# Performance work log

Hardware: AMD Instinct MI355X
Metric: run time of the kernel (lower is better)

The kernel has to match this reference:

```python
import jax, jax.numpy as jnp
import numpy as np

N = 50000   # n_nodes (cells)
E = 800000  # n_edges (avg degree 16)
D = 128     # feature dim


def setup_inputs() -> dict:
    key = jax.random.key(0)
    ks = jax.random.split(key, 8)
    x = jax.random.normal(ks[0], (N, D), dtype=jnp.float32)
    src = jax.random.randint(ks[1], (E,), 0, N, dtype=jnp.int32)
    dst = jax.random.randint(ks[2], (E,), 0, N, dtype=jnp.int32)
    vals = jax.random.uniform(ks[3], (E,), dtype=jnp.float32)
    # GraphConvolution weight (dim -> dim), applied as x @ W
    W_gc = jax.random.normal(ks[4], (D, D), dtype=jnp.float32) / np.sqrt(D).astype(np.float32)
    b_gc = jnp.zeros((D,), jnp.float32)
    # linear2: nn.Linear(dim, dim) -> x @ W2.T + b2
    W2 = jax.random.normal(ks[5], (D, D), dtype=jnp.float32) / np.sqrt(D).astype(np.float32)
    b2 = jnp.zeros((D,), jnp.float32)
    return {"x": x, "vals": vals, "W_gc": W_gc, "b_gc": b_gc,
            "W2": W2, "b2": b2, "src": src, "dst": dst}


def reference(x, vals, W_gc, b_gc, W2, b2, src, dst):
    # GraphConvolution (dropout is identity in eval mode):
    #   support = x @ W + b ; out = relu(adj_sparse @ support)
    support = x @ W_gc + b_gc                         # [N, D]
    msg = support[src] * vals[:, None]                # gather rows, scale by edge weight
    agg = jax.ops.segment_sum(msg, dst, num_segments=N)  # SpMM via scatter-add
    x1 = jax.nn.relu(agg)                             # [N, D]
    # linear2 + dropout(eval=identity) + detached L2 row-normalize
    x2 = x1 @ W2.T + b2                               # [N, D]
    nrm = jax.lax.stop_gradient(
        jnp.sqrt(jnp.sum(x2 * x2, axis=1, keepdims=True)))
    return x2 / nrm
```

## Files before the change

### kernel.cpp

```cpp
#include <hip/hip_runtime.h>
#include <hip/hip_bf16.h>

#define N_NODES 50000
#define N_EDGES 800000
#define DIM     128
#define N_STRIPS (N_NODES / 16)
#define N_BKT    782
#define EDGE_CHUNKS 196
#define BCAP     1536
#define EBUF_CAP 1408
#define AGS      68
#define GEMM_BLOCKS ((N_STRIPS + 3) / 4)
#define FRONT_BLOCKS (GEMM_BLOCKS + EDGE_CHUNKS)

typedef short short8 __attribute__((ext_vector_type(8)));
typedef float floatx4 __attribute__((ext_vector_type(4)));

__device__ inline unsigned short f2bf(float f) {
    __hip_bfloat16 h = __float2bfloat16(f);
    return *reinterpret_cast<unsigned short*>(&h);
}

__global__ __launch_bounds__(256) void pre_pack(
    const float* __restrict__ W1, const float* __restrict__ W2,
    uint4* __restrict__ p1, uint4* __restrict__ p2, int* __restrict__ bcnt)
{
    const int blk = blockIdx.x;
    const int t   = threadIdx.x;
    if (blk < 8) {
        const int s    = blk * 256 + t;
        const int lane = s & 63;
        const int nt   = (s >> 6) & 7;
        const int ks   = s >> 9;
        const int m    = lane & 15;
        const int q    = lane >> 4;
        unsigned short e[8];
        #pragma unroll
        for (int j = 0; j < 8; ++j)
            e[j] = f2bf(W1[(ks * 32 + q * 8 + j) * DIM + nt * 16 + m]);
        uint4 o;
        o.x = (unsigned)e[0] | ((unsigned)e[1] << 16);
        o.y = (unsigned)e[2] | ((unsigned)e[3] << 16);
        o.z = (unsigned)e[4] | ((unsigned)e[5] << 16);
        o.w = (unsigned)e[6] | ((unsigned)e[7] << 16);
        p1[s] = o;
    } else if (blk < 16) {
        const int s    = (blk - 8) * 256 + t;
        const int lane = s & 63;
        const int nt   = (s >> 6) & 7;
        const int ks   = s >> 9;
        const int m    = lane & 15;
        const int q    = lane >> 4;
        const float4 f0 = *reinterpret_cast<const float4*>(&W2[(nt * 16 + m) * DIM + ks * 32 + q * 8]);
        const float4 f1 = *reinterpret_cast<const float4*>(&W2[(nt * 16 + m) * DIM + ks * 32 + q * 8 + 4]);
        unsigned short e[8];
        e[0] = f2bf(f0.x); e[1] = f2bf(f0.y); e[2] = f2bf(f0.z); e[3] = f2bf(f0.w);
        e[4] = f2bf(f1.x); e[5] = f2bf(f1.y); e[6] = f2bf(f1.z); e[7] = f2bf(f1.w);
        uint4 o;
        o.x = (unsigned)e[0] | ((unsigned)e[1] << 16);
        o.y = (unsigned)e[2] | ((unsigned)e[3] << 16);
        o.z = (unsigned)e[4] | ((unsigned)e[5] << 16);
        o.w = (unsigned)e[6] | ((unsigned)e[7] << 16);
        p2[s] = o;
    } else {
        for (int i = t; i < 800; i += 256) bcnt[i] = 0;
    }
}

__global__ __launch_bounds__(256) void front(
    const float* __restrict__ x, const float* __restrict__ bias,
    const int* __restrict__ src, const int* __restrict__ dst,
    const float* __restrict__ vals, const uint4* __restrict__ p1,
    unsigned short* __restrict__ support, int* __restrict__ bcnt,
    int2* __restrict__ bucketed)
{
    __shared__ int bh[800];
    __shared__ int rcur[800];
    const int t = threadIdx.x;

    if (blockIdx.x < EDGE_CHUNKS) {
        const int chunk = blockIdx.x;
        for (int i = t; i < 800; i += 256) bh[i] = 0;
        __syncthreads();
        const int base   = chunk * 4096;
        const int navail = min(4096, N_EDGES - base);
        const int4* d4 = reinterpret_cast<const int4*>(dst + base);
        #pragma unroll
        for (int i = 0; i < 4; ++i) {
            const int j = t + i * 256;
            if (j * 4 < navail) {
                const int4 d = d4[j];
                atomicAdd(&bh[d.x >> 6], 1);
                atomicAdd(&bh[d.y >> 6], 1);
                atomicAdd(&bh[d.z >> 6], 1);
                atomicAdd(&bh[d.w >> 6], 1);
            }
        }
        __syncthreads();
        for (int b = t; b < N_BKT; b += 256)
            rcur[b] = b * BCAP + atomicAdd(&bcnt[b], bh[b]);
        __syncthreads();
        const int4*   s4 = reinterpret_cast<const int4*>(src + base);
        const float4* v4 = reinterpret_cast<const float4*>(vals + base);
        #pragma unroll
        for (int i = 0; i < 4; ++i) {
            const int j = t + i * 256;
            if (j * 4 < navail) {
                const int4   s = s4[j];
                const int4   d = d4[j];
                const float4 v = v4[j];
                int p;
                p = atomicAdd(&rcur[d.x >> 6], 1);
                bucketed[p] = make_int2((s.x & 0xFFFF) | ((d.x & 63) << 16), __float_as_int(v.x));
                p = atomicAdd(&rcur[d.y >> 6], 1);
                bucketed[p] = make_int2((s.y & 0xFFFF) | ((d.y & 63) << 16), __float_as_int(v.y));
                p = atomicAdd(&rcur[d.z >> 6], 1);
                bucketed[p] = make_int2((s.z & 0xFFFF) | ((d.z & 63) << 16), __float_as_int(v.z));
                p = atomicAdd(&rcur[d.w >> 6], 1);
                bucketed[p] = make_int2((s.w & 0xFFFF) | ((d.w & 63) << 16), __float_as_int(v.w));
            }
        }
    } else {
        const int wave  = t >> 6;
        const int lane  = t & 63;
        const int strip = (blockIdx.x - EDGE_CHUNKS) * 4 + wave;
        if (strip >= N_STRIPS) return;
        const int m = lane & 15;
        const int q = lane >> 4;
        const int row = strip * 16 + m;

        short8 a[4];
        const float4* xr = reinterpret_cast<const float4*>(&x[(size_t)row * DIM]);
        #pragma unroll
        for (int ks = 0; ks < 4; ++ks) {
            const float4 f0 = xr[ks * 8 + q * 2];
            const float4 f1 = xr[ks * 8 + q * 2 + 1];
            short8 tt;
            tt[0] = (short)f2bf(f0.x); tt[1] = (short)f2bf(f0.y);
            tt[2] = (short)f2bf(f0.z); tt[3] = (short)f2bf(f0.w);
            tt[4] = (short)f2bf(f1.x); tt[5] = (short)f2bf(f1.y);
            tt[6] = (short)f2bf(f1.z); tt[7] = (short)f2bf(f1.w);
            a[ks] = tt;
        }

        floatx4 acc[8];
        #pragma unroll
        for (int nt = 0; nt < 8; ++nt) { acc[nt][0]=0.f; acc[nt][1]=0.f; acc[nt][2]=0.f; acc[nt][3]=0.f; }

        const short8* Bp = (const short8*)p1;
        #pragma unroll
        for (int ks = 0; ks < 4; ++ks) {
            #pragma unroll
            for (int nt = 0; nt < 8; ++nt) {
                const short8 bf = Bp[(ks * 8 + nt) * 64 + lane];
                acc[nt] = __builtin_amdgcn_mfma_f32_16x16x32_bf16(a[ks], bf, acc[nt], 0, 0, 0);
            }
        }

        #pragma unroll
        for (int nt = 0; nt < 8; ++nt) {
            const float bb = bias[nt * 16 + m];
            #pragma unroll
            for (int i = 0; i < 4; ++i) {
                const int r = strip * 16 + q * 4 + i;
                support[(size_t)r * DIM + nt * 16 + m] = f2bf(acc[nt][i] + bb);
            }
        }
    }
}

__global__ __launch_bounds__(256) void agg_gemm2(
    const unsigned int* __restrict__ sup, const int2* __restrict__ bucketed,
    const int* __restrict__ bcnt, const short8* __restrict__ Bp,
    const float* __restrict__ bias, float* __restrict__ out)
{
    __shared__ int2 ebuf[EBUF_CAP];
    __shared__ unsigned int agg[64 * AGS];
    __shared__ int cnt[64];
    __shared__ int coff[64];
    __shared__ int cur[64];

    const int b = blockIdx.x;
    const int t = threadIdx.x;
    int nE = bcnt[b];
    if (nE > EBUF_CAP) nE = EBUF_CAP;
    const int base = b * BCAP;

    if (t < 64) cnt[t] = 0;
    __syncthreads();
    for (int i = t; i < nE; i += 256)
        atomicAdd(&cnt[(bucketed[base + i].x >> 16) & 63], 1);
    __syncthreads();
    if (t < 64) coff[t] = cnt[t];
    __syncthreads();
    for (int off = 1; off < 64; off <<= 1) {
        int u = 0;
        if (t < 64 && t >= off) u = coff[t - off];
        __syncthreads();
        if (t < 64 && t >= off) coff[t] += u;
        __syncthreads();
    }
    if (t < 64) cur[t] = coff[t] - cnt[t];
    __syncthreads();
    for (int i = t; i < nE; i += 256) {
        const int2 e = bucketed[base + i];
        const int  n = (e.x >> 16) & 63;
        const int  p = atomicAdd(&cur[n], 1);
        ebuf[p] = e;
    }
    __syncthreads();

    const int w    = t >> 6;
    const int lane = t & 63;
    const int g    = lane >> 4;
    const int dl   = lane & 15;

    for (int nl = w * 16; nl < w * 16 + 16; ++nl) {
        const int end = cur[nl];
        const int c   = cnt[nl];
        const int beg = end - c;
        float acc[8];
        #pragma unroll
        for (int k = 0; k < 8; ++k) acc[k] = 0.f;

        const int nI = (c + 3) >> 2;
        auto step = [&](int it) {
            const int  idx = beg + it * 4 + g;
            const bool vld = idx < end;
            const int2 e   = ebuf[vld ? idx : beg];
            const float val = vld ? __int_as_float(e.y) : 0.f;
            const uint4 u = *reinterpret_cast<const uint4*>(
                &sup[(size_t)(e.x & 0xFFFF) * 64 + dl * 4]);
            acc[0] += __uint_as_float(u.x << 16)          * val;
            acc[1] += __uint_as_float(u.x & 0xffff0000u)  * val;
            acc[2] += __uint_as_float(u.y << 16)          * val;
            acc[3] += __uint_as_float(u.y & 0xffff0000u)  * val;
            acc[4] += __uint_as_float(u.z << 16)          * val;
            acc[5] += __uint_as_float(u.z & 0xffff0000u)  * val;
            acc[6] += __uint_as_float(u.w << 16)          * val;
            acc[7] += __uint_as_float(u.w & 0xffff0000u)  * val;
        };
        int it = 0;
        for (; it + 3 < nI; it += 4) { step(it); step(it+1); step(it+2); step(it+3); }
        for (; it < nI; ++it) step(it);

        #pragma unroll
        for (int k = 0; k < 8; ++k) {
            acc[k] += __shfl_xor(acc[k], 16);
            acc[k] += __shfl_xor(acc[k], 32);
        }
        if (dl == lane) {
            uint4 o;
            o.x = (unsigned)f2bf(fmaxf(acc[0],0.f)) | ((unsigned)f2bf(fmaxf(acc[1],0.f)) << 16);
            o.y = (unsigned)f2bf(fmaxf(acc[2],0.f)) | ((unsigned)f2bf(fmaxf(acc[3],0.f)) << 16);
            o.z = (unsigned)f2bf(fmaxf(acc[4],0.f)) | ((unsigned)f2bf(fmaxf(acc[5],0.f)) << 16);
            o.w = (unsigned)f2bf(fmaxf(acc[6],0.f)) | ((unsigned)f2bf(fmaxf(acc[7],0.f)) << 16);
            *reinterpret_cast<uint4*>(&agg[nl * AGS + dl * 4]) = o;
        }
    }
    __syncthreads();

    const int row0 = b * 64 + w * 16;
    if (row0 >= N_NODES) return;
    const int m = lane & 15;
    const int q = lane >> 4;

    short8 a[4];
    #pragma unroll
    for (int ks = 0; ks < 4; ++ks) {
        const uint4 t4 = *reinterpret_cast<const uint4*>(&agg[(w * 16 + m) * AGS + ks * 16 + q * 4]);
        a[ks] = *reinterpret_cast<const short8*>(&t4);
    }

    floatx4 acc[8];
    #pragma unroll
    for (int nt = 0; nt < 8; ++nt) { acc[nt][0]=0.f; acc[nt][1]=0.f; acc[nt][2]=0.f; acc[nt][3]=0.f; }

    #pragma unroll
    for (int ks = 0; ks < 4; ++ks) {
        #pragma unroll
        for (int nt = 0; nt < 8; ++nt) {
            const short8 bf = Bp[(ks * 8 + nt) * 64 + lane];
            acc[nt] = __builtin_amdgcn_mfma_f32_16x16x32_bf16(a[ks], bf, acc[nt], 0, 0, 0);
        }
    }

    #pragma unroll
    for (int nt = 0; nt < 8; ++nt) {
        const float bb = bias[nt * 16 + m];
        #pragma unroll
        for (int i = 0; i < 4; ++i) acc[nt][i] += bb;
    }

    float sq[4] = {0.f, 0.f, 0.f, 0.f};
    #pragma unroll
    for (int nt = 0; nt < 8; ++nt)
        #pragma unroll
        for (int i = 0; i < 4; ++i) sq[i] += acc[nt][i] * acc[nt][i];
    #pragma unroll
    for (int i = 0; i < 4; ++i) {
        #pragma unroll
        for (int mask = 1; mask < 16; mask <<= 1)
            sq[i] += __shfl_xor(sq[i], mask);
        sq[i] = 1.0f / sqrtf(sq[i]);
    }

    #pragma unroll
    for (int nt = 0; nt < 8; ++nt) {
        #pragma unroll
        for (int i = 0; i < 4; ++i) {
            const int r = row0 + q * 4 + i;
            out[(size_t)r * DIM + nt * 16 + m] = acc[nt][i] * sq[i];
        }
    }
}

extern "C" void kernel_launch(void* const* d_in, const int* in_sizes, int n_in,
                              void* d_out, int out_size, void* d_ws, size_t ws_size,
                              hipStream_t stream) {
    const float* x    = (const float*)d_in[0];
    const float* vals = (const float*)d_in[1];
    const float* W_gc = (const float*)d_in[2];
    const float* b_gc = (const float*)d_in[3];
    const float* W2   = (const float*)d_in[4];
    const float* b2   = (const float*)d_in[5];
    const int*   src  = (const int*)d_in[6];
    const int*   dst  = (const int*)d_in[7];

    float* out = (float*)d_out;

    const size_t SUP_B = (size_t)N_NODES * DIM * 2;
    const size_t BUK_B = (size_t)N_BKT * BCAP * 8;
    char* wsb = (char*)d_ws;
    unsigned short* support = (unsigned short*)wsb;
    int2* bucketed = (int2*)(wsb + SUP_B);
    int*  bcnt     = (int*)(wsb + SUP_B + BUK_B);
    uint4* pw1     = (uint4*)(wsb + SUP_B + BUK_B + 4096);
    uint4* pw2     = (uint4*)(wsb + SUP_B + BUK_B + 4096 + 32768);

    pre_pack<<<17, 256, 0, stream>>>(W_gc, W2, pw1, pw2, bcnt);

    front<<<FRONT_BLOCKS, 256, 0, stream>>>(
        x, b_gc, src, dst, vals, pw1, support, bcnt, bucketed);

    agg_gemm2<<<N_BKT, 256, 0, stream>>>(
        (const unsigned int*)support, bucketed, bcnt, (const short8*)pw2, b2, out);
}
```

Baseline: 148.4 us.

## Split SpMM gather into two feature-half kernels and stage support writes through LDS

The aggregation is split into two passes, each gathering only one 64-feature half of the bf16 support rows. The first pass writes its half to a global buffer, and the second computes its half and then runs the second GEMM. The intent is to halve the gathered working set per pass so it fits better in cache, and to process two nodes per wave with 8-lane groups for more memory-level parallelism. The first GEMM now stages its output tile in LDS so global stores are coalesced, and edge chunks are doubled to 8192 edges. In exchange the edge bucket sort is done twice, one more kernel is launched, and there is an extra global round trip for the first half of the aggregation.

```diff
diff --git a/kernel.cpp b/kernel.cpp
--- a/kernel.cpp
+++ b/kernel.cpp
@@ -6,12 +6,13 @@
 #define DIM     128
 #define N_STRIPS (N_NODES / 16)
 #define N_BKT    782
-#define EDGE_CHUNKS 196
+#define CHUNK_E  8192
+#define EDGE_CHUNKS ((N_EDGES + CHUNK_E - 1) / CHUNK_E)
 #define BCAP     1536
 #define EBUF_CAP 1408
-#define AGS      68
 #define GEMM_BLOCKS ((N_STRIPS + 3) / 4)
-#define FRONT_BLOCKS (GEMM_BLOCKS + EDGE_CHUNKS)
+#define FRONT_BLOCKS (EDGE_CHUNKS + GEMM_BLOCKS)
+#define SUP_ROWS 50048
 
 typedef short short8 __attribute__((ext_vector_type(8)));
 typedef float floatx4 __attribute__((ext_vector_type(4)));
@@ -19,6 +20,15 @@
 __device__ inline unsigned short f2bf(float f) {
     __hip_bfloat16 h = __float2bfloat16(f);
     return *reinterpret_cast<unsigned short*>(&h);
+}
+
+__device__ inline uint4 pack8_relu(const float a[8]) {
+    uint4 o;
+    o.x = (unsigned)f2bf(fmaxf(a[0],0.f)) | ((unsigned)f2bf(fmaxf(a[1],0.f)) << 16);
+    o.y = (unsigned)f2bf(fmaxf(a[2],0.f)) | ((unsigned)f2bf(fmaxf(a[3],0.f)) << 16);
+    o.z = (unsigned)f2bf(fmaxf(a[4],0.f)) | ((unsigned)f2bf(fmaxf(a[5],0.f)) << 16);
+    o.w = (unsigned)f2bf(fmaxf(a[6],0.f)) | ((unsigned)f2bf(fmaxf(a[7],0.f)) << 16);
+    return o;
 }
 
 __global__ __launch_bounds__(256) void pre_pack(
@@ -76,17 +86,18 @@
 {
     __shared__ int bh[800];
     __shared__ int rcur[800];
+    __shared__ unsigned short stg[64 * 136];
     const int t = threadIdx.x;
 
     if (blockIdx.x < EDGE_CHUNKS) {
         const int chunk = blockIdx.x;
         for (int i = t; i < 800; i += 256) bh[i] = 0;
         __syncthreads();
-        const int base   = chunk * 4096;
-        const int navail = min(4096, N_EDGES - base);
+        const int base   = chunk * CHUNK_E;
+        const int navail = min(CHUNK_E, N_EDGES - base);
         const int4* d4 = reinterpret_cast<const int4*>(dst + base);
         #pragma unroll
-        for (int i = 0; i < 4; ++i) {
+        for (int i = 0; i < 8; ++i) {
             const int j = t + i * 256;
             if (j * 4 < navail) {
                 const int4 d = d4[j];
@@ -103,7 +114,7 @@
         const int4*   s4 = reinterpret_cast<const int4*>(src + base);
         const float4* v4 = reinterpret_cast<const float4*>(vals + base);
         #pragma unroll
-        for (int i = 0; i < 4; ++i) {
+        for (int i = 0; i < 8; ++i) {
             const int j = t + i * 256;
             if (j * 4 < navail) {
                 const int4   s = s4[j];
@@ -121,61 +132,70 @@
             }
         }
     } else {
+        const int gb    = blockIdx.x - EDGE_CHUNKS;
         const int wave  = t >> 6;
         const int lane  = t & 63;
-        const int strip = (blockIdx.x - EDGE_CHUNKS) * 4 + wave;
-        if (strip >= N_STRIPS) return;
+        const int strip = gb * 4 + wave;
         const int m = lane & 15;
         const int q = lane >> 4;
-        const int row = strip * 16 + m;
-
-        short8 a[4];
-        const float4* xr = reinterpret_cast<const float4*>(&x[(size_t)row * DIM]);
-        #pragma unroll
-        for (int ks = 0; ks < 4; ++ks) {
-            const float4 f0 = xr[ks * 8 + q * 2];
-            const float4 f1 = xr[ks * 8 + q * 2 + 1];
-            short8 tt;
-            tt[0] = (short)f2bf(f0.x); tt[1] = (short)f2bf(f0.y);
-            tt[2] = (short)f2bf(f0.z); tt[3] = (short)f2bf(f0.w);
-            tt[4] = (short)f2bf(f1.x); tt[5] = (short)f2bf(f1.y);
-            tt[6] = (short)f2bf(f1.z); tt[7] = (short)f2bf(f1.w);
-            a[ks] = tt;
-        }
-
-        floatx4 acc[8];
-        #pragma unroll
-        for (int nt = 0; nt < 8; ++nt) { acc[nt][0]=0.f; acc[nt][1]=0.f; acc[nt][2]=0.f; acc[nt][3]=0.f; }
-
-        const short8* Bp = (const short8*)p1;
-        #pragma unroll
-        for (int ks = 0; ks < 4; ++ks) {
+        const bool valid = strip < N_STRIPS;
+
+        if (valid) {
+            const int row = strip * 16 + m;
+            short8 a[4];
+            const float4* xr = reinterpret_cast<const float4*>(&x[(size_t)row * DIM]);
+            #pragma unroll
+            for (int ks = 0; ks < 4; ++ks) {
+                const float4 f0 = xr[ks * 8 + q * 2];
+                const float4 f1 = xr[ks * 8 + q * 2 + 1];
+                short8 tt;
+                tt[0] = (short)f2bf(f0.x); tt[1] = (short)f2bf(f0.y);
+                tt[2] = (short)f2bf(f0.z); tt[3] = (short)f2bf(f0.w);
+                tt[4] = (short)f2bf(f1.x); tt[5] = (short)f2bf(f1.y);
+                tt[6] = (short)f2bf(f1.z); tt[7] = (short)f2bf(f1.w);
+                a[ks] = tt;
+            }
+
+            floatx4 acc[8];
+            #pragma unroll
+            for (int nt = 0; nt < 8; ++nt) { acc[nt][0]=0.f; acc[nt][1]=0.f; acc[nt][2]=0.f; acc[nt][3]=0.f; }
+
+            const short8* Bp = (const short8*)p1;
+            #pragma unroll
+            for (int ks = 0; ks < 4; ++ks) {
+                #pragma unroll
+                for (int nt = 0; nt < 8; ++nt) {
+                    const short8 bf = Bp[(ks * 8 + nt) * 64 + lane];
+                    acc[nt] = __builtin_amdgcn_mfma_f32_16x16x32_bf16(a[ks], bf, acc[nt], 0, 0, 0);
+                }
+            }
+
             #pragma unroll
             for (int nt = 0; nt < 8; ++nt) {
-                const short8 bf = Bp[(ks * 8 + nt) * 64 + lane];
-                acc[nt] = __builtin_amdgcn_mfma_f32_16x16x32_bf16(a[ks], bf, acc[nt], 0, 0, 0);
+                const float bb = bias[nt * 16 + m];
+                #pragma unroll
+                for (int i = 0; i < 4; ++i)
+                    stg[(wave * 16 + q * 4 + i) * 136 + nt * 16 + m] = f2bf(acc[nt][i] + bb);
             }
         }
-
-        #pragma unroll
-        for (int nt = 0; nt < 8; ++nt) {
-            const float bb = bias[nt * 16 + m];
-            #pragma unroll
-            for (int i = 0; i < 4; ++i) {
-                const int r = strip * 16 + q * 4 + i;
-                support[(size_t)r * DIM + nt * 16 + m] = f2bf(acc[nt][i] + bb);
-            }
-        }
-    }
-}
-
-__global__ __launch_bounds__(256) void agg_gemm2(
+        __syncthreads();
+        const size_t rbase = (size_t)gb * 64;
+        #pragma unroll
+        for (int k = 0; k < 4; ++k) {
+            const int chunk2 = t + k * 256;
+            const int lrow  = chunk2 >> 4;
+            const int piece = chunk2 & 15;
+            const uint4 v = *reinterpret_cast<const uint4*>(&stg[lrow * 136 + piece * 8]);
+            *reinterpret_cast<uint4*>(&support[(rbase + lrow) * DIM + piece * 8]) = v;
+        }
+    }
+}
+
+__global__ __launch_bounds__(256) void gather_h0(
     const unsigned int* __restrict__ sup, const int2* __restrict__ bucketed,
-    const int* __restrict__ bcnt, const short8* __restrict__ Bp,
-    const float* __restrict__ bias, float* __restrict__ out)
+    const int* __restrict__ bcnt, unsigned int* __restrict__ aggG)
 {
     __shared__ int2 ebuf[EBUF_CAP];
-    __shared__ unsigned int agg[64 * AGS];
     __shared__ int cnt[64];
     __shared__ int coff[64];
     __shared__ int cur[64];
@@ -210,52 +230,160 @@
     }
     __syncthreads();
 
-    const int w    = t >> 6;
-    const int lane = t & 63;
-    const int g    = lane >> 4;
-    const int dl   = lane & 15;
-
-    for (int nl = w * 16; nl < w * 16 + 16; ++nl) {
-        const int end = cur[nl];
-        const int c   = cnt[nl];
-        const int beg = end - c;
-        float acc[8];
-        #pragma unroll
-        for (int k = 0; k < 8; ++k) acc[k] = 0.f;
-
-        const int nI = (c + 3) >> 2;
-        auto step = [&](int it) {
-            const int  idx = beg + it * 4 + g;
-            const bool vld = idx < end;
-            const int2 e   = ebuf[vld ? idx : beg];
-            const float val = vld ? __int_as_float(e.y) : 0.f;
-            const uint4 u = *reinterpret_cast<const uint4*>(
-                &sup[(size_t)(e.x & 0xFFFF) * 64 + dl * 4]);
-            acc[0] += __uint_as_float(u.x << 16)          * val;
-            acc[1] += __uint_as_float(u.x & 0xffff0000u)  * val;
-            acc[2] += __uint_as_float(u.y << 16)          * val;
-            acc[3] += __uint_as_float(u.y & 0xffff0000u)  * val;
-            acc[4] += __uint_as_float(u.z << 16)          * val;
-            acc[5] += __uint_as_float(u.z & 0xffff0000u)  * val;
-            acc[6] += __uint_as_float(u.w << 16)          * val;
-            acc[7] += __uint_as_float(u.w & 0xffff0000u)  * val;
-        };
-        int it = 0;
-        for (; it + 3 < nI; it += 4) { step(it); step(it+1); step(it+2); step(it+3); }
-        for (; it < nI; ++it) step(it);
-
+    const int w = t >> 6, lane = t & 63;
+    const int g = lane >> 3, dl = lane & 7;
+    for (int j = 0; j < 8; ++j) {
+        const int nA = w * 16 + j, nB = nA + 8;
+        const int endA = cur[nA], cA = cnt[nA], begA = endA - cA;
+        const int endB = cur[nB], cB = cnt[nB], begB = endB - cB;
+        float aA[8] = {0.f,0.f,0.f,0.f,0.f,0.f,0.f,0.f};
+        float aB[8] = {0.f,0.f,0.f,0.f,0.f,0.f,0.f,0.f};
+        const int nI = max((cA + 7) >> 3, (cB + 7) >> 3);
+        #pragma unroll 2
+        for (int it = 0; it < nI; ++it) {
+            const int iA = begA + it * 8 + g;
+            const int iB = begB + it * 8 + g;
+            const bool vA = iA < endA, vB = iB < endB;
+            const int2 eA = ebuf[vA ? iA : 0];
+            const int2 eB = ebuf[vB ? iB : 0];
+            const float valA = vA ? __int_as_float(eA.y) : 0.f;
+            const float valB = vB ? __int_as_float(eB.y) : 0.f;
+            const int sA = vA ? (eA.x & 0xFFFF) : 0;
+            const int sB = vB ? (eB.x & 0xFFFF) : 0;
+            const uint4 uA = *reinterpret_cast<const uint4*>(&sup[(size_t)sA * 64 + dl * 4]);
+            const uint4 uB = *reinterpret_cast<const uint4*>(&sup[(size_t)sB * 64 + dl * 4]);
+            aA[0] += __uint_as_float(uA.x << 16)         * valA;
+            aA[1] += __uint_as_float(uA.x & 0xffff0000u) * valA;
+            aA[2] += __uint_as_float(uA.y << 16)         * valA;
+            aA[3] += __uint_as_float(uA.y & 0xffff0000u) * valA;
+            aA[4] += __uint_as_float(uA.z << 16)         * valA;
+            aA[5] += __uint_as_float(uA.z & 0xffff0000u) * valA;
+            aA[6] += __uint_as_float(uA.w << 16)         * valA;
+            aA[7] += __uint_as_float(uA.w & 0xffff0000u) * valA;
+            aB[0] += __uint_as_float(uB.x << 16)         * valB;
+            aB[1] += __uint_as_float(uB.x & 0xffff0000u) * valB;
+            aB[2] += __uint_as_float(uB.y << 16)         * valB;
+            aB[3] += __uint_as_float(uB.y & 0xffff0000u) * valB;
+            aB[4] += __uint_as_float(uB.z << 16)         * valB;
+            aB[5] += __uint_as_float(uB.z & 0xffff0000u) * valB;
+            aB[6] += __uint_as_float(uB.w << 16)         * valB;
+            aB[7] += __uint_as_float(uB.w & 0xffff0000u) * valB;
+        }
         #pragma unroll
         for (int k = 0; k < 8; ++k) {
-            acc[k] += __shfl_xor(acc[k], 16);
-            acc[k] += __shfl_xor(acc[k], 32);
-        }
-        if (dl == lane) {
-            uint4 o;
-            o.x = (unsigned)f2bf(fmaxf(acc[0],0.f)) | ((unsigned)f2bf(fmaxf(acc[1],0.f)) << 16);
-            o.y = (unsigned)f2bf(fmaxf(acc[2],0.f)) | ((unsigned)f2bf(fmaxf(acc[3],0.f)) << 16);
-            o.z = (unsigned)f2bf(fmaxf(acc[4],0.f)) | ((unsigned)f2bf(fmaxf(acc[5],0.f)) << 16);
-            o.w = (unsigned)f2bf(fmaxf(acc[6],0.f)) | ((unsigned)f2bf(fmaxf(acc[7],0.f)) << 16);
-            *reinterpret_cast<uint4*>(&agg[nl * AGS + dl * 4]) = o;
+            aA[k] += __shfl_xor(aA[k], 8);
+            aA[k] += __shfl_xor(aA[k], 16);
+            aA[k] += __shfl_xor(aA[k], 32);
+            aB[k] += __shfl_xor(aB[k], 8);
+            aB[k] += __shfl_xor(aB[k], 16);
+            aB[k] += __shfl_xor(aB[k], 32);
+        }
+        if (lane < 8) {
+            const uint4 oA = pack8_relu(aA);
+            const uint4 oB = pack8_relu(aB);
+            const int nodeA = b * 64 + nA;
+            const int nodeB = b * 64 + nB;
+            if (nodeA < N_NODES)
+                *reinterpret_cast<uint4*>(&aggG[(size_t)nodeA * 32 + lane * 4]) = oA;
+            if (nodeB < N_NODES)
+                *reinterpret_cast<uint4*>(&aggG[(size_t)nodeB * 32 + lane * 4]) = oB;
+        }
+    }
+}
+
+__global__ __launch_bounds__(256) void gather_h1_gemm2(
+    const unsigned int* __restrict__ sup, const int2* __restrict__ bucketed,
+    const int* __restrict__ bcnt, const unsigned int* __restrict__ aggG,
+    const short8* __restrict__ Bp, const float* __restrict__ bias,
+    float* __restrict__ out)
+{
+    __shared__ int2 ebuf[EBUF_CAP];
+    __shared__ unsigned int aggL[64 * 36];
+    __shared__ int cnt[64];
+    __shared__ int coff[64];
+    __shared__ int cur[64];
+
+    const int b = blockIdx.x;
+    const int t = threadIdx.x;
+    int nE = bcnt[b];
+    if (nE > EBUF_CAP) nE = EBUF_CAP;
+    const int base = b * BCAP;
+
+    if (t < 64) cnt[t] = 0;
+    __syncthreads();
+    for (int i = t; i < nE; i += 256)
+        atomicAdd(&cnt[(bucketed[base + i].x >> 16) & 63], 1);
+    __syncthreads();
+    if (t < 64) coff[t] = cnt[t];
+    __syncthreads();
+    for (int off = 1; off < 64; off <<= 1) {
+        int u = 0;
+        if (t < 64 && t >= off) u = coff[t - off];
+        __syncthreads();
+        if (t < 64 && t >= off) coff[t] += u;
+        __syncthreads();
+    }
+    if (t < 64) cur[t] = coff[t] - cnt[t];
+    __syncthreads();
+    for (int i = t; i < nE; i += 256) {
+        const int2 e = bucketed[base + i];
+        const int  n = (e.x >> 16) & 63;
+        const int  p = atomicAdd(&cur[n], 1);
+        ebuf[p] = e;
+    }
+    __syncthreads();
+
+    const int w = t >> 6, lane = t & 63;
+    const int g = lane >> 3, dl = lane & 7;
+    for (int j = 0; j < 8; ++j) {
+        const int nA = w * 16 + j, nB = nA + 8;
+        const int endA = cur[nA], cA = cnt[nA], begA = endA - cA;
+        const int endB = cur[nB], cB = cnt[nB], begB = endB - cB;
+        float aA[8] = {0.f,0.f,0.f,0.f,0.f,0.f,0.f,0.f};
+        float aB[8] = {0.f,0.f,0.f,0.f,0.f,0.f,0.f,0.f};
+        const int nI = max((cA + 7) >> 3, (cB + 7) >> 3);
+        #pragma unroll 2
+        for (int it = 0; it < nI; ++it) {
+            const int iA = begA + it * 8 + g;
+            const int iB = begB + it * 8 + g;
+            const bool vA = iA < endA, vB = iB < endB;
+            const int2 eA = ebuf[vA ? iA : 0];
+            const int2 eB = ebuf[vB ? iB : 0];
+            const float valA = vA ? __int_as_float(eA.y) : 0.f;
+            const float valB = vB ? __int_as_float(eB.y) : 0.f;
+            const int sA = vA ? (eA.x & 0xFFFF) : 0;
+            const int sB = vB ? (eB.x & 0xFFFF) : 0;
+            const uint4 uA = *reinterpret_cast<const uint4*>(&sup[(size_t)sA * 64 + 32 + dl * 4]);
+            const uint4 uB = *reinterpret_cast<const uint4*>(&sup[(size_t)sB * 64 + 32 + dl * 4]);
+            aA[0] += __uint_as_float(uA.x << 16)         * valA;
+            aA[1] += __uint_as_float(uA.x & 0xffff0000u) * valA;
+            aA[2] += __uint_as_float(uA.y << 16)         * valA;
+            aA[3] += __uint_as_float(uA.y & 0xffff0000u) * valA;
+            aA[4] += __uint_as_float(uA.z << 16)         * valA;
+            aA[5] += __uint_as_float(uA.z & 0xffff0000u) * valA;
+            aA[6] += __uint_as_float(uA.w << 16)         * valA;
+            aA[7] += __uint_as_float(uA.w & 0xffff0000u) * valA;
+            aB[0] += __uint_as_float(uB.x << 16)         * valB;
+            aB[1] += __uint_as_float(uB.x & 0xffff0000u) * valB;
+            aB[2] += __uint_as_float(uB.y << 16)         * valB;
+            aB[3] += __uint_as_float(uB.y & 0xffff0000u) * valB;
+            aB[4] += __uint_as_float(uB.z << 16)         * valB;
+            aB[5] += __uint_as_float(uB.z & 0xffff0000u) * valB;
+            aB[6] += __uint_as_float(uB.w << 16)         * valB;
+            aB[7] += __uint_as_float(uB.w & 0xffff0000u) * valB;
+        }
+        #pragma unroll
+        for (int k = 0; k < 8; ++k) {
+            aA[k] += __shfl_xor(aA[k], 8);
+            aA[k] += __shfl_xor(aA[k], 16);
+            aA[k] += __shfl_xor(aA[k], 32);
+            aB[k] += __shfl_xor(aB[k], 8);
+            aB[k] += __shfl_xor(aB[k], 16);
+            aB[k] += __shfl_xor(aB[k], 32);
+        }
+        if (lane < 8) {
+            *reinterpret_cast<uint4*>(&aggL[nA * 36 + lane * 4]) = pack8_relu(aA);
+            *reinterpret_cast<uint4*>(&aggL[nB * 36 + lane * 4]) = pack8_relu(aB);
         }
     }
     __syncthreads();
@@ -264,11 +392,17 @@
     if (row0 >= N_NODES) return;
     const int m = lane & 15;
     const int q = lane >> 4;
+    const int grow = row0 + m;
 
     short8 a[4];
     #pragma unroll
-    for (int ks = 0; ks < 4; ++ks) {
-        const uint4 t4 = *reinterpret_cast<const uint4*>(&agg[(w * 16 + m) * AGS + ks * 16 + q * 4]);
+    for (int ks = 0; ks < 2; ++ks) {
+        const uint4 t4 = *reinterpret_cast<const uint4*>(&aggG[(size_t)grow * 32 + ks * 16 + q * 4]);
+        a[ks] = *reinterpret_cast<const short8*>(&t4);
+    }
+    #pragma unroll
+    for (int ks = 2; ks < 4; ++ks) {
+        const uint4 t4 = *reinterpret_cast<const uint4*>(&aggL[(w * 16 + m) * 36 + (ks - 2) * 16 + q * 4]);
         a[ks] = *reinterpret_cast<const short8*>(&t4);
     }
 
@@ -329,20 +463,26 @@
 
     float* out = (float*)d_out;
 
-    const size_t SUP_B = (size_t)N_NODES * DIM * 2;
+    const size_t SUP_B = (size_t)SUP_ROWS * DIM * 2;
     const size_t BUK_B = (size_t)N_BKT * BCAP * 8;
+    const size_t AGG_B = (size_t)SUP_ROWS * 64 * 2;
     char* wsb = (char*)d_ws;
     unsigned short* support = (unsigned short*)wsb;
     int2* bucketed = (int2*)(wsb + SUP_B);
-    int*  bcnt     = (int*)(wsb + SUP_B + BUK_B);
-    uint4* pw1     = (uint4*)(wsb + SUP_B + BUK_B + 4096);
-    uint4* pw2     = (uint4*)(wsb + SUP_B + BUK_B + 4096 + 32768);
+    unsigned int* aggG = (unsigned int*)(wsb + SUP_B + BUK_B);
+    int*  bcnt     = (int*)(wsb + SUP_B + BUK_B + AGG_B);
+    uint4* pw1     = (uint4*)(wsb + SUP_B + BUK_B + AGG_B + 4096);
+    uint4* pw2     = (uint4*)(wsb + SUP_B + BUK_B + AGG_B + 4096 + 32768);
 
     pre_pack<<<17, 256, 0, stream>>>(W_gc, W2, pw1, pw2, bcnt);
 
     front<<<FRONT_BLOCKS, 256, 0, stream>>>(
         x, b_gc, src, dst, vals, pw1, support, bcnt, bucketed);
 
-    agg_gemm2<<<N_BKT, 256, 0, stream>>>(
-        (const unsigned int*)support, bucketed, bcnt, (const short8*)pw2, b2, out);
-}
+    gather_h0<<<N_BKT, 256, 0, stream>>>(
+        (const unsigned int*)support, bucketed, bcnt, aggG);
+
+    gather_h1_gemm2<<<N_BKT, 256, 0, stream>>>(
+        (const unsigned int*)support, bucketed, bcnt, aggG,
+        (const short8*)pw2, b2, out);
+}
```

Result: slower. 168.7 us (+13.7%).

## Fuse weight packing into front kernel and widen aggregation blocks to 512 threads

Applied to the files above, without the earlier changes.

Removes the separate pre_pack launch. Each GEMM block now converts W1 into an LDS-resident packed bf16 layout itself, and W2 packing is folded into extra blocks of the fused front kernel. The bucket-count reset moves to a hipMemsetAsync. Support rows are staged through LDS so global stores are coalesced 16-byte writes.

The aggregation kernel doubles to 512 threads, so each wave handles 8 nodes instead of 16, and only the first four waves run the second GEMM. This trades a kernel launch and strided stores for redundant per-block W1 conversion work and an added memset.

```diff
diff --git a/kernel.cpp b/kernel.cpp
--- a/kernel.cpp
+++ b/kernel.cpp
@@ -6,12 +6,14 @@
 #define DIM     128
 #define N_STRIPS (N_NODES / 16)
 #define N_BKT    782
+#define CHUNK_E  4096
 #define EDGE_CHUNKS 196
 #define BCAP     1536
 #define EBUF_CAP 1408
+#define GEMM_BLOCKS 782
+#define D1_BLOCKS (EDGE_CHUNKS + GEMM_BLOCKS + 8)
+#define SUP_ROWS 50048
 #define AGS      68
-#define GEMM_BLOCKS ((N_STRIPS + 3) / 4)
-#define FRONT_BLOCKS (GEMM_BLOCKS + EDGE_CHUNKS)
 
 typedef short short8 __attribute__((ext_vector_type(8)));
 typedef float floatx4 __attribute__((ext_vector_type(4)));
@@ -21,31 +23,150 @@
     return *reinterpret_cast<unsigned short*>(&h);
 }
 
-__global__ __launch_bounds__(256) void pre_pack(
-    const float* __restrict__ W1, const float* __restrict__ W2,
-    uint4* __restrict__ p1, uint4* __restrict__ p2, int* __restrict__ bcnt)
+__device__ inline uint4 pack8_relu(const float a[8]) {
+    uint4 o;
+    o.x = (unsigned)f2bf(fmaxf(a[0],0.f)) | ((unsigned)f2bf(fmaxf(a[1],0.f)) << 16);
+    o.y = (unsigned)f2bf(fmaxf(a[2],0.f)) | ((unsigned)f2bf(fmaxf(a[3],0.f)) << 16);
+    o.z = (unsigned)f2bf(fmaxf(a[4],0.f)) | ((unsigned)f2bf(fmaxf(a[5],0.f)) << 16);
+    o.w = (unsigned)f2bf(fmaxf(a[6],0.f)) | ((unsigned)f2bf(fmaxf(a[7],0.f)) << 16);
+    return o;
+}
+
+__global__ __launch_bounds__(256) void fused1(
+    const float* __restrict__ x, const float* __restrict__ W1,
+    const float* __restrict__ bias, const float* __restrict__ W2,
+    const int* __restrict__ src, const int* __restrict__ dst,
+    const float* __restrict__ vals,
+    unsigned short* __restrict__ support, int* __restrict__ bcnt,
+    int2* __restrict__ bucketed, uint4* __restrict__ p2)
 {
-    const int blk = blockIdx.x;
-    const int t   = threadIdx.x;
-    if (blk < 8) {
-        const int s    = blk * 256 + t;
-        const int lane = s & 63;
-        const int nt   = (s >> 6) & 7;
-        const int ks   = s >> 9;
-        const int m    = lane & 15;
-        const int q    = lane >> 4;
-        unsigned short e[8];
-        #pragma unroll
-        for (int j = 0; j < 8; ++j)
-            e[j] = f2bf(W1[(ks * 32 + q * 8 + j) * DIM + nt * 16 + m]);
-        uint4 o;
-        o.x = (unsigned)e[0] | ((unsigned)e[1] << 16);
-        o.y = (unsigned)e[2] | ((unsigned)e[3] << 16);
-        o.z = (unsigned)e[4] | ((unsigned)e[5] << 16);
-        o.w = (unsigned)e[6] | ((unsigned)e[7] << 16);
-        p1[s] = o;
-    } else if (blk < 16) {
-        const int s    = (blk - 8) * 256 + t;
+    __shared__ __align__(16) char smem[32768];
+    const int t = threadIdx.x;
+
+    if (blockIdx.x < EDGE_CHUNKS) {
+        int* bh   = (int*)smem;
+        int* rcur = (int*)smem + 800;
+        const int chunk = blockIdx.x;
+        for (int i = t; i < 800; i += 256) bh[i] = 0;
+        __syncthreads();
+        const int base   = chunk * CHUNK_E;
+        const int navail = min(CHUNK_E, N_EDGES - base);
+        const int4* d4 = reinterpret_cast<const int4*>(dst + base);
+        #pragma unroll
+        for (int i = 0; i < 4; ++i) {
+            const int j = t + i * 256;
+            if (j * 4 < navail) {
+                const int4 d = d4[j];
+                atomicAdd(&bh[d.x >> 6], 1);
+                atomicAdd(&bh[d.y >> 6], 1);
+                atomicAdd(&bh[d.z >> 6], 1);
+                atomicAdd(&bh[d.w >> 6], 1);
+            }
+        }
+        __syncthreads();
+        for (int b = t; b < N_BKT; b += 256)
+            rcur[b] = b * BCAP + atomicAdd(&bcnt[b], bh[b]);
+        __syncthreads();
+        const int4*   s4 = reinterpret_cast<const int4*>(src + base);
+        const float4* v4 = reinterpret_cast<const float4*>(vals + base);
+        #pragma unroll
+        for (int i = 0; i < 4; ++i) {
+            const int j = t + i * 256;
+            if (j * 4 < navail) {
+                const int4   s = s4[j];
+                const int4   d = d4[j];
+                const float4 v = v4[j];
+                int p;
+                p = atomicAdd(&rcur[d.x >> 6], 1);
+                bucketed[p] = make_int2((s.x & 0xFFFF) | ((d.x & 63) << 16), __float_as_int(v.x));
+                p = atomicAdd(&rcur[d.y >> 6], 1);
+                bucketed[p] = make_int2((s.y & 0xFFFF) | ((d.y & 63) << 16), __float_as_int(v.y));
+                p = atomicAdd(&rcur[d.z >> 6], 1);
+                bucketed[p] = make_int2((s.z & 0xFFFF) | ((d.z & 63) << 16), __float_as_int(v.z));
+                p = atomicAdd(&rcur[d.w >> 6], 1);
+                bucketed[p] = make_int2((s.w & 0xFFFF) | ((d.w & 63) << 16), __float_as_int(v.w));
+            }
+        }
+    } else if (blockIdx.x < EDGE_CHUNKS + GEMM_BLOCKS) {
+        const int gb    = blockIdx.x - EDGE_CHUNKS;
+        const int wave  = t >> 6;
+        const int lane  = t & 63;
+        const int strip = gb * 4 + wave;
+        const int m = lane & 15;
+        const int q = lane >> 4;
+        const bool valid = strip < N_STRIPS;
+
+        unsigned short* w1e = (unsigned short*)smem;
+        #pragma unroll
+        for (int i = 0; i < 16; ++i) {
+            const int f4 = t + i * 256;
+            const float4 v = reinterpret_cast<const float4*>(W1)[f4];
+            const float vv[4] = {v.x, v.y, v.z, v.w};
+            const int e0 = f4 * 4;
+            #pragma unroll
+            for (int j = 0; j < 4; ++j) {
+                const int k = (e0 + j) >> 7, n = (e0 + j) & 127;
+                const int ks = k >> 5, qq = (k >> 3) & 3, jj = k & 7;
+                const int nt = n >> 4, mm = n & 15;
+                w1e[((ks * 8 + nt) * 64 + qq * 16 + mm) * 8 + jj] = f2bf(vv[j]);
+            }
+        }
+        __syncthreads();
+
+        floatx4 acc[8];
+        #pragma unroll
+        for (int nt = 0; nt < 8; ++nt) { acc[nt][0]=0.f; acc[nt][1]=0.f; acc[nt][2]=0.f; acc[nt][3]=0.f; }
+
+        if (valid) {
+            const int row = strip * 16 + m;
+            short8 a[4];
+            const float4* xr = reinterpret_cast<const float4*>(&x[(size_t)row * DIM]);
+            #pragma unroll
+            for (int ks = 0; ks < 4; ++ks) {
+                const float4 f0 = xr[ks * 8 + q * 2];
+                const float4 f1 = xr[ks * 8 + q * 2 + 1];
+                short8 tt;
+                tt[0] = (short)f2bf(f0.x); tt[1] = (short)f2bf(f0.y);
+                tt[2] = (short)f2bf(f0.z); tt[3] = (short)f2bf(f0.w);
+                tt[4] = (short)f2bf(f1.x); tt[5] = (short)f2bf(f1.y);
+                tt[6] = (short)f2bf(f1.z); tt[7] = (short)f2bf(f1.w);
+                a[ks] = tt;
+            }
+            const short8* w1f = (const short8*)smem;
+            #pragma unroll
+            for (int ks = 0; ks < 4; ++ks) {
+                #pragma unroll
+                for (int nt = 0; nt < 8; ++nt) {
+                    const short8 bf = w1f[(ks * 8 + nt) * 64 + lane];
+                    acc[nt] = __builtin_amdgcn_mfma_f32_16x16x32_bf16(a[ks], bf, acc[nt], 0, 0, 0);
+                }
+            }
+        }
+        __syncthreads();
+
+        unsigned short* stg = (unsigned short*)smem;
+        if (valid) {
+            #pragma unroll
+            for (int nt = 0; nt < 8; ++nt) {
+                const float bb = bias[nt * 16 + m];
+                #pragma unroll
+                for (int i = 0; i < 4; ++i)
+                    stg[(wave * 16 + q * 4 + i) * 136 + nt * 16 + m] = f2bf(acc[nt][i] + bb);
+            }
+        }
+        __syncthreads();
+        const size_t rbase = (size_t)gb * 64;
+        #pragma unroll
+        for (int k2 = 0; k2 < 4; ++k2) {
+            const int chunk2 = t + k2 * 256;
+            const int lrow  = chunk2 >> 4;
+            const int piece = chunk2 & 15;
+            const uint4 v = *reinterpret_cast<const uint4*>(&stg[lrow * 136 + piece * 8]);
+            *reinterpret_cast<uint4*>(&support[(rbase + lrow) * DIM + piece * 8]) = v;
+        }
+    } else {
+        const int pb   = blockIdx.x - (EDGE_CHUNKS + GEMM_BLOCKS);
+        const int s    = pb * 256 + t;
         const int lane = s & 63;
         const int nt   = (s >> 6) & 7;
         const int ks   = s >> 9;
@@ -62,114 +183,10 @@
         o.z = (unsigned)e[4] | ((unsigned)e[5] << 16);
         o.w = (unsigned)e[6] | ((unsigned)e[7] << 16);
         p2[s] = o;
-    } else {
-        for (int i = t; i < 800; i += 256) bcnt[i] = 0;
-    }
-}
-
-__global__ __launch_bounds__(256) void front(
-    const float* __restrict__ x, const float* __restrict__ bias,
-    const int* __restrict__ src, const int* __restrict__ dst,
-    const float* __restrict__ vals, const uint4* __restrict__ p1,
-    unsigned short* __restrict__ support, int* __restrict__ bcnt,
-    int2* __restrict__ bucketed)
-{
-    __shared__ int bh[800];
-    __shared__ int rcur[800];
-    const int t = threadIdx.x;
-
-    if (blockIdx.x < EDGE_CHUNKS) {
-        const int chunk = blockIdx.x;
-        for (int i = t; i < 800; i += 256) bh[i] = 0;
-        __syncthreads();
-        const int base   = chunk * 4096;
-        const int navail = min(4096, N_EDGES - base);
-        const int4* d4 = reinterpret_cast<const int4*>(dst + base);
-        #pragma unroll
-        for (int i = 0; i < 4; ++i) {
-            const int j = t + i * 256;
-            if (j * 4 < navail) {
-                const int4 d = d4[j];
-                atomicAdd(&bh[d.x >> 6], 1);
-                atomicAdd(&bh[d.y >> 6], 1);
-                atomicAdd(&bh[d.z >> 6], 1);
-                atomicAdd(&bh[d.w >> 6], 1);
-            }
-        }
-        __syncthreads();
-        for (int b = t; b < N_BKT; b += 256)
-            rcur[b] = b * BCAP + atomicAdd(&bcnt[b], bh[b]);
-        __syncthreads();
-        const int4*   s4 = reinterpret_cast<const int4*>(src + base);
-        const float4* v4 = reinterpret_cast<const float4*>(vals + base);
-        #pragma unroll
-        for (int i = 0; i < 4; ++i) {
-            const int j = t + i * 256;
-            if (j * 4 < navail) {
-                const int4   s = s4[j];
-                const int4   d = d4[j];
-                const float4 v = v4[j];
-                int p;
-                p = atomicAdd(&rcur[d.x >> 6], 1);
-                bucketed[p] = make_int2((s.x & 0xFFFF) | ((d.x & 63) << 16), __float_as_int(v.x));
-                p = atomicAdd(&rcur[d.y >> 6], 1);
-                bucketed[p] = make_int2((s.y & 0xFFFF) | ((d.y & 63) << 16), __float_as_int(v.y));
-                p = atomicAdd(&rcur[d.z >> 6], 1);
-                bucketed[p] = make_int2((s.z & 0xFFFF) | ((d.z & 63) << 16), __float_as_int(v.z));
-                p = atomicAdd(&rcur[d.w >> 6], 1);
-                bucketed[p] = make_int2((s.w & 0xFFFF) | ((d.w & 63) << 16), __float_as_int(v.w));
-            }
-        }
-    } else {
-        const int wave  = t >> 6;
-        const int lane  = t & 63;
-        const int strip = (blockIdx.x - EDGE_CHUNKS) * 4 + wave;
-        if (strip >= N_STRIPS) return;
-        const int m = lane & 15;
-        const int q = lane >> 4;
-        const int row = strip * 16 + m;
-
-        short8 a[4];
-        const float4* xr = reinterpret_cast<const float4*>(&x[(size_t)row * DIM]);
-        #pragma unroll
-        for (int ks = 0; ks < 4; ++ks) {
-            const float4 f0 = xr[ks * 8 + q * 2];
-            const float4 f1 = xr[ks * 8 + q * 2 + 1];
-            short8 tt;
-            tt[0] = (short)f2bf(f0.x); tt[1] = (short)f2bf(f0.y);
-            tt[2] = (short)f2bf(f0.z); tt[3] = (short)f2bf(f0.w);
-            tt[4] = (short)f2bf(f1.x); tt[5] = (short)f2bf(f1.y);
-            tt[6] = (short)f2bf(f1.z); tt[7] = (short)f2bf(f1.w);
-            a[ks] = tt;
-        }
-
-        floatx4 acc[8];
-        #pragma unroll
-        for (int nt = 0; nt < 8; ++nt) { acc[nt][0]=0.f; acc[nt][1]=0.f; acc[nt][2]=0.f; acc[nt][3]=0.f; }
-
-        const short8* Bp = (const short8*)p1;
-        #pragma unroll
-        for (int ks = 0; ks < 4; ++ks) {
-            #pragma unroll
-            for (int nt = 0; nt < 8; ++nt) {
-                const short8 bf = Bp[(ks * 8 + nt) * 64 + lane];
-                acc[nt] = __builtin_amdgcn_mfma_f32_16x16x32_bf16(a[ks], bf, acc[nt], 0, 0, 0);
-            }
-        }
-
-        #pragma unroll
-        for (int nt = 0; nt < 8; ++nt) {
-            const float bb = bias[nt * 16 + m];
-            #pragma unroll
-            for (int i = 0; i < 4; ++i) {
-                const int r = strip * 16 + q * 4 + i;
-                support[(size_t)r * DIM + nt * 16 + m] = f2bf(acc[nt][i] + bb);
-            }
-        }
-    }
-}
-
-__global__ __launch_bounds__(256) void agg_gemm2(
+    }
+}
+
+__global__ __launch_bounds__(512) void agg_gemm2(
     const unsigned int* __restrict__ sup, const int2* __restrict__ bucketed,
     const int* __restrict__ bcnt, const short8* __restrict__ Bp,
     const float* __restrict__ bias, float* __restrict__ out)
@@ -188,7 +205,7 @@
 
     if (t < 64) cnt[t] = 0;
     __syncthreads();
-    for (int i = t; i < nE; i += 256)
+    for (int i = t; i < nE; i += 512)
         atomicAdd(&cnt[(bucketed[base + i].x >> 16) & 63], 1);
     __syncthreads();
     if (t < 64) coff[t] = cnt[t];
@@ -202,7 +219,7 @@
     }
     if (t < 64) cur[t] = coff[t] - cnt[t];
     __syncthreads();
-    for (int i = t; i < nE; i += 256) {
+    for (int i = t; i < nE; i += 512) {
         const int2 e = bucketed[base + i];
         const int  n = (e.x >> 16) & 63;
         const int  p = atomicAdd(&cur[n], 1);
@@ -215,7 +232,7 @@
     const int g    = lane >> 4;
     const int dl   = lane & 15;
 
-    for (int nl = w * 16; nl < w * 16 + 16; ++nl) {
+    for (int nl = w * 8; nl < w * 8 + 8; ++nl) {
         const int end = cur[nl];
         const int c   = cnt[nl];
         const int beg = end - c;
@@ -249,17 +266,13 @@
             acc[k] += __shfl_xor(acc[k], 16);
             acc[k] += __shfl_xor(acc[k], 32);
         }
-        if (dl == lane) {
-            uint4 o;
-            o.x = (unsigned)f2bf(fmaxf(acc[0],0.f)) | ((unsigned)f2bf(fmaxf(acc[1],0.f)) << 16);
-            o.y = (unsigned)f2bf(fmaxf(acc[2],0.f)) | ((unsigned)f2bf(fmaxf(acc[3],0.f)) << 16);
-            o.z = (unsigned)f2bf(fmaxf(acc[4],0.f)) | ((unsigned)f2bf(fmaxf(acc[5],0.f)) << 16);
-            o.w = (unsigned)f2bf(fmaxf(acc[6],0.f)) | ((unsigned)f2bf(fmaxf(acc[7],0.f)) << 16);
-            *reinterpret_cast<uint4*>(&agg[nl * AGS + dl * 4]) = o;
-        }
-    }
-    __syncthreads();
-
+        if (lane < 16) {
+            *reinterpret_cast<uint4*>(&agg[nl * AGS + dl * 4]) = pack8_relu(acc);
+        }
+    }
+    __syncthreads();
+
+    if (w >= 4) return;
     const int row0 = b * 64 + w * 16;
     if (row0 >= N_NODES) return;
     const int m = lane & 15;
@@ -329,20 +342,19 @@
 
     float* out = (float*)d_out;
 
-    const size_t SUP_B = (size_t)N_NODES * DIM * 2;
+    const size_t SUP_B = (size_t)SUP_ROWS * DIM * 2;
     const size_t BUK_B = (size_t)N_BKT * BCAP * 8;
     char* wsb = (char*)d_ws;
     unsigned short* support = (unsigned short*)wsb;
-    int2* bucketed = (int2*)(wsb + SUP_B);
-    int*  bcnt     = (int*)(wsb + SUP_B + BUK_B);
-    uint4* pw1     = (uint4*)(wsb + SUP_B + BUK_B + 4096);
-    uint4* pw2     = (uint4*)(wsb + SUP_B + BUK_B + 4096 + 32768);
-
-    pre_pack<<<17, 256, 0, stream>>>(W_gc, W2, pw1, pw2, bcnt);
-
-    front<<<FRONT_BLOCKS, 256, 0, stream>>>(
-        x, b_gc, src, dst, vals, pw1, support, bcnt, bucketed);
-
-    agg_gemm2<<<N_BKT, 256, 0, stream>>>(
+    int2*  bucketed = (int2*)(wsb + SUP_B);
+    int*   bcnt     = (int*)(wsb + SUP_B + BUK_B);
+    uint4* pw2      = (uint4*)(wsb + SUP_B + BUK_B + 4096);
+
+    hipMemsetAsync(bcnt, 0, 800 * sizeof(int), stream);
+
+    fused1<<<D1_BLOCKS, 256, 0, stream>>>(
+        x, W_gc, b_gc, W2, src, dst, vals, support, bcnt, bucketed, pw2);
+
+    agg_gemm2<<<N_BKT, 512, 0, stream>>>(
         (const unsigned int*)support, bucketed, bcnt, (const short8*)pw2, b2, out);
 }
```

After: 156.8 us. 5.7% more time.
